# Kernel tuning notes

Measured on AMD Instinct MI355X. Metric: run time of the kernel, lower is better.

The kernel has to match this reference:

```python
import jax, jax.numpy as jnp
import numpy as np

ALPHA = 0.2          # LeakyReLU negative slope
NEG_BIG = -9e15      # mask fill value from the original code
N, IN_F, OUT_F = 8192, 128, 64


def setup_inputs() -> dict:
    key = jax.random.key(0)
    k1, k2, k3, k4 = jax.random.split(key, 4)
    h = jax.random.normal(k1, (N, IN_F), dtype=jnp.float32)
    adj = jax.random.randint(k2, (N, N), 0, 2, dtype=jnp.int32)
    W = jax.random.normal(k3, (IN_F, OUT_F), dtype=jnp.float32) * 0.1
    a = jax.random.normal(k4, (2 * OUT_F, 1), dtype=jnp.float32) * 0.1
    return {"h": h, "adj": adj, "W": W, "a": a}


def reference(h, adj, W, a):
    # Wh: [N, F]
    Wh = h @ W
    # e_ij = leakyrelu([Wh_i ; Wh_j] . a) = leakyrelu(Wh_i.a1 + Wh_j.a2)
    # (identical math to the original NxNx2F concat, without materializing it)
    a1 = a[:OUT_F, 0]   # [F]
    a2 = a[OUT_F:, 0]   # [F]
    s1 = Wh @ a1        # [N]
    s2 = Wh @ a2        # [N]
    e = jax.nn.leaky_relu(s1[:, None] + s2[None, :], negative_slope=ALPHA)  # [N, N]
    e = jnp.where(adj > 0, e, jnp.float32(NEG_BIG))
    attention = jax.nn.softmax(e, axis=1)
    # dropout is identity at inference (training=False)
    h_prime = attention @ Wh  # [N, F]
    return jax.nn.elu(h_prime)  # concat=True -> elu
```

## Files before the change

kernel.cpp:

```cpp
#include <hip/hip_runtime.h>
#include <hip/hip_bf16.h>

#define N 8192
#define IN_F 128
#define OUT_F 64
#define LRELU_ALPHA 0.2f
#define PAD 520

typedef __attribute__((ext_vector_type(8))) short short8;
typedef __attribute__((ext_vector_type(4))) float float4v;
typedef __attribute__((ext_vector_type(4))) unsigned short ushortx4;

__device__ __forceinline__ unsigned short bf16_bits(float x) {
  unsigned u = __builtin_bit_cast(unsigned, x);
  u += 0x7fffu + ((u >> 16) & 1u);
  return (unsigned short)(u >> 16);
}

__global__ __launch_bounds__(256) void prep_kernel(
    const float* __restrict__ h, const float* __restrict__ W,
    const float* __restrict__ a, float* __restrict__ s1,
    float* __restrict__ s2, unsigned short* __restrict__ whT) {
  const int tid = threadIdx.x;
  const int row = blockIdx.x * 4 + (tid >> 6);
  const int k = tid & 63;
  const float* hr = h + row * IN_F;
  float acc = 0.f;
#pragma unroll 8
  for (int c = 0; c < IN_F; ++c) acc = fmaf(hr[c], W[c * OUT_F + k], acc);
  whT[(long)k * N + row] = bf16_bits(acc);
  float p1 = acc * a[k];
  float p2 = acc * a[OUT_F + k];
#pragma unroll
  for (int off = 32; off > 0; off >>= 1) {
    p1 += __shfl_xor(p1, off);
    p2 += __shfl_xor(p2, off);
  }
  if (k == 0) { s1[row] = p1; s2[row] = p2; }
}

__global__ __launch_bounds__(256) void repack_kernel(
    const unsigned short* __restrict__ whT, unsigned short* __restrict__ whF) {
  const int f = blockIdx.x * 256 + threadIdx.x;
  const int lane = f & 63, tt = (f >> 6) & 3, c = f >> 8;
  const int r16 = lane & 15, quad = lane >> 4;
  const short8 v = *(const short8*)(whT + (long)(tt * 16 + r16) * N + c * 32 + quad * 8);
  *(short8*)(whF + (long)f * 8) = v;
}

__device__ __forceinline__ void p_write(unsigned short* pr, int c, int4 av,
                                        float4 s2v, float s1w) {
  float e0 = s1w + s2v.x; e0 = fmaxf(e0, LRELU_ALPHA * e0);
  float e1 = s1w + s2v.y; e1 = fmaxf(e1, LRELU_ALPHA * e1);
  float e2 = s1w + s2v.z; e2 = fmaxf(e2, LRELU_ALPHA * e2);
  float e3 = s1w + s2v.w; e3 = fmaxf(e3, LRELU_ALPHA * e3);
  const float p0 = av.x > 0 ? __expf(e0) : 0.f;
  const float p1 = av.y > 0 ? __expf(e1) : 0.f;
  const float p2 = av.z > 0 ? __expf(e2) : 0.f;
  const float p3 = av.w > 0 ? __expf(e3) : 0.f;
  ushortx4 pk = {bf16_bits(p0), bf16_bits(p1), bf16_bits(p2), bf16_bits(p3)};
  *(ushortx4*)(pr + c) = pk;
}

__global__ __launch_bounds__(1024, 4) void gat_kernel(
    const int* __restrict__ adj, const float* __restrict__ s1,
    const float* __restrict__ s2, const unsigned short* __restrict__ whF,
    float* __restrict__ out) {
  __shared__ __align__(16) unsigned short pbuf[2][16][PAD];
  const int tid = threadIdx.x;
  const int w = tid >> 6, L = tid & 63;
  const int r16 = L & 15, quad = L >> 4;
  const int row0 = blockIdx.x * 16;
  const long arow = (long)(row0 + w) * N;
  const float s1w = s1[row0 + w];

  float4v acc0 = {0.f, 0.f, 0.f, 0.f};
  float4v acc1 = {0.f, 0.f, 0.f, 0.f};
  float4v acc2 = {0.f, 0.f, 0.f, 0.f};
  float4v acc3 = {0.f, 0.f, 0.f, 0.f};
  float4v accD = {0.f, 0.f, 0.f, 0.f};
  const short ONE = (short)0x3F80;
  const short8 ones = {ONE, ONE, ONE, ONE, ONE, ONE, ONE, ONE};

  {
    const int c = L * 4;
    const int4 a0 = *(const int4*)(adj + arow + c);
    const int4 a1 = *(const int4*)(adj + arow + 256 + c);
    const float4 sv0 = *(const float4*)(s2 + c);
    const float4 sv1 = *(const float4*)(s2 + 256 + c);
    p_write(pbuf[0][w], c, a0, sv0, s1w);
    p_write(pbuf[0][w], 256 + c, a1, sv1, s1w);
  }
  __syncthreads();

  for (int it = 0; it < 16; ++it) {
    const int b = it & 1;
    int4 na0, na1;
    float4 ns0, ns1;
    if (it < 15) {
      const long base = arow + (it + 1) * 512 + L * 4;
      na0 = *(const int4*)(adj + base);
      na1 = *(const int4*)(adj + base + 256);
      ns0 = *(const float4*)(s2 + (it + 1) * 512 + L * 4);
      ns1 = *(const float4*)(s2 + (it + 1) * 512 + 256 + L * 4);
    }
    const int c32 = it * 16 + w;
    const short8 afrag = *(const short8*)(&pbuf[b][r16][w * 32 + quad * 8]);
    const unsigned short* bp = whF + ((long)c32 * 256 + L) * 8;
    const short8 b0 = *(const short8*)(bp);
    const short8 b1 = *(const short8*)(bp + 512);
    const short8 b2 = *(const short8*)(bp + 1024);
    const short8 b3 = *(const short8*)(bp + 1536);
    acc0 = __builtin_amdgcn_mfma_f32_16x16x32_bf16(afrag, b0, acc0, 0, 0, 0);
    acc1 = __builtin_amdgcn_mfma_f32_16x16x32_bf16(afrag, b1, acc1, 0, 0, 0);
    acc2 = __builtin_amdgcn_mfma_f32_16x16x32_bf16(afrag, b2, acc2, 0, 0, 0);
    acc3 = __builtin_amdgcn_mfma_f32_16x16x32_bf16(afrag, b3, acc3, 0, 0, 0);
    accD = __builtin_amdgcn_mfma_f32_16x16x32_bf16(afrag, ones, accD, 0, 0, 0);
    if (it < 15) {
      unsigned short* pr = pbuf[b ^ 1][w];
      const int c = L * 4;
      p_write(pr, c, na0, ns0, s1w);
      p_write(pr, 256 + c, na1, ns1, s1w);
    }
    __syncthreads();
  }

  float* M = (float*)pbuf;
  if (w >= 8) {
    float* S = M + (w - 8) * 1040;
#pragma unroll
    for (int reg = 0; reg < 4; ++reg) {
      const int r = quad * 4 + reg;
      S[r * 64 + 0 * 16 + r16] = acc0[reg];
      S[r * 64 + 1 * 16 + r16] = acc1[reg];
      S[r * 64 + 2 * 16 + r16] = acc2[reg];
      S[r * 64 + 3 * 16 + r16] = acc3[reg];
      if (r16 == 0) S[1024 + r] = accD[reg];
    }
  }
  __syncthreads();
  if (w < 8) {
    float* S = M + w * 1040;
#pragma unroll
    for (int reg = 0; reg < 4; ++reg) {
      const int r = quad * 4 + reg;
      S[r * 64 + 0 * 16 + r16] += acc0[reg];
      S[r * 64 + 1 * 16 + r16] += acc1[reg];
      S[r * 64 + 2 * 16 + r16] += acc2[reg];
      S[r * 64 + 3 * 16 + r16] += acc3[reg];
      if (r16 == 0) S[1024 + r] += accD[reg];
    }
  }
  __syncthreads();
  {
    const int r = tid >> 6, k = tid & 63;
    float Sv = 0.f, Lv = 0.f;
#pragma unroll
    for (int s = 0; s < 8; ++s) {
      Sv += M[s * 1040 + r * 64 + k];
      Lv += M[s * 1040 + 1024 + r];
    }
    const float v = Sv / Lv;
    out[(long)(row0 + r) * OUT_F + k] = v > 0.f ? v : expm1f(v);
  }
}

extern "C" void kernel_launch(void* const* d_in, const int* in_sizes, int n_in,
                              void* d_out, int out_size, void* d_ws, size_t ws_size,
                              hipStream_t stream) {
  const float* h = (const float*)d_in[0];
  const int* adj = (const int*)d_in[1];
  const float* W = (const float*)d_in[2];
  const float* a = (const float*)d_in[3];
  float* out = (float*)d_out;

  float* s1 = (float*)d_ws;
  float* s2 = s1 + N;
  unsigned short* whT = (unsigned short*)(s2 + N);
  unsigned short* whF = whT + (long)OUT_F * N;

  prep_kernel<<<N / 4, 256, 0, stream>>>(h, W, a, s1, s2, whT);
  repack_kernel<<<N * OUT_F / 8 / 256, 256, 0, stream>>>(whT, whF);
  gat_kernel<<<N / 16, 1024, 0, stream>>>(adj, s1, s2, whF, out);
}
```

Baseline: 392.1 us.

## Halve gat block size, two rows per wave, deeper adj prefetch

The GAT kernel now launches 512 threads per block, and each wave handles two attention rows and two K-chunks per iteration. Adjacency loads are prefetched two iterations ahead through a register ring so more HBM traffic is in flight per wave. The final reduction across waves is adapted to 8 waves with 4 partial slices. The prep kernel also reads h rows as float4. The cost is more live registers per thread, which may lower occupancy.

```diff
diff --git a/kernel.cpp b/kernel.cpp
--- a/kernel.cpp
+++ b/kernel.cpp
@@ -24,10 +24,17 @@
   const int tid = threadIdx.x;
   const int row = blockIdx.x * 4 + (tid >> 6);
   const int k = tid & 63;
-  const float* hr = h + row * IN_F;
+  const float4* hr4 = (const float4*)(h + row * IN_F);
   float acc = 0.f;
-#pragma unroll 8
-  for (int c = 0; c < IN_F; ++c) acc = fmaf(hr[c], W[c * OUT_F + k], acc);
+#pragma unroll
+  for (int c4 = 0; c4 < IN_F / 4; ++c4) {
+    const float4 hv = hr4[c4];
+    const int cb = c4 * 4;
+    acc = fmaf(hv.x, W[(cb + 0) * OUT_F + k], acc);
+    acc = fmaf(hv.y, W[(cb + 1) * OUT_F + k], acc);
+    acc = fmaf(hv.z, W[(cb + 2) * OUT_F + k], acc);
+    acc = fmaf(hv.w, W[(cb + 3) * OUT_F + k], acc);
+  }
   whT[(long)k * N + row] = bf16_bits(acc);
   float p1 = acc * a[k];
   float p2 = acc * a[OUT_F + k];
@@ -62,7 +69,7 @@
   *(ushortx4*)(pr + c) = pk;
 }
 
-__global__ __launch_bounds__(1024, 4) void gat_kernel(
+__global__ __launch_bounds__(512, 4) void gat_kernel(
     const int* __restrict__ adj, const float* __restrict__ s1,
     const float* __restrict__ s2, const unsigned short* __restrict__ whF,
     float* __restrict__ out) {
@@ -71,8 +78,12 @@
   const int w = tid >> 6, L = tid & 63;
   const int r16 = L & 15, quad = L >> 4;
   const int row0 = blockIdx.x * 16;
-  const long arow = (long)(row0 + w) * N;
-  const float s1w = s1[row0 + w];
+  const int rA = 2 * w, rB = 2 * w + 1;
+  const long arowA = (long)(row0 + rA) * N;
+  const long arowB = (long)(row0 + rB) * N;
+  const float s1A = s1[row0 + rA];
+  const float s1B = s1[row0 + rB];
+  const int c = L * 4;
 
   float4v acc0 = {0.f, 0.f, 0.f, 0.f};
   float4v acc1 = {0.f, 0.f, 0.f, 0.f};
@@ -82,52 +93,77 @@
   const short ONE = (short)0x3F80;
   const short8 ones = {ONE, ONE, ONE, ONE, ONE, ONE, ONE, ONE};
 
+  int4 pA0[2], pA1[2], pB0[2], pB1[2];
+  float4 ps0, ps1;
+
   {
-    const int c = L * 4;
-    const int4 a0 = *(const int4*)(adj + arow + c);
-    const int4 a1 = *(const int4*)(adj + arow + 256 + c);
+    const int4 a0 = *(const int4*)(adj + arowA + c);
+    const int4 a1 = *(const int4*)(adj + arowA + 256 + c);
+    const int4 b0 = *(const int4*)(adj + arowB + c);
+    const int4 b1 = *(const int4*)(adj + arowB + 256 + c);
     const float4 sv0 = *(const float4*)(s2 + c);
     const float4 sv1 = *(const float4*)(s2 + 256 + c);
-    p_write(pbuf[0][w], c, a0, sv0, s1w);
-    p_write(pbuf[0][w], 256 + c, a1, sv1, s1w);
+    pA0[0] = *(const int4*)(adj + arowA + 512 + c);
+    pA1[0] = *(const int4*)(adj + arowA + 512 + 256 + c);
+    pB0[0] = *(const int4*)(adj + arowB + 512 + c);
+    pB1[0] = *(const int4*)(adj + arowB + 512 + 256 + c);
+    pA0[1] = *(const int4*)(adj + arowA + 1024 + c);
+    pA1[1] = *(const int4*)(adj + arowA + 1024 + 256 + c);
+    pB0[1] = *(const int4*)(adj + arowB + 1024 + c);
+    pB1[1] = *(const int4*)(adj + arowB + 1024 + 256 + c);
+    ps0 = *(const float4*)(s2 + 512 + c);
+    ps1 = *(const float4*)(s2 + 512 + 256 + c);
+    p_write(pbuf[0][rA], c, a0, sv0, s1A);
+    p_write(pbuf[0][rA], 256 + c, a1, sv1, s1A);
+    p_write(pbuf[0][rB], c, b0, sv0, s1B);
+    p_write(pbuf[0][rB], 256 + c, b1, sv1, s1B);
   }
   __syncthreads();
 
+#pragma unroll
   for (int it = 0; it < 16; ++it) {
     const int b = it & 1;
-    int4 na0, na1;
-    float4 ns0, ns1;
+    const int s = it & 1;
+#pragma unroll
+    for (int half = 0; half < 2; ++half) {
+      const int cc = w + half * 8;
+      const short8 afrag = *(const short8*)(&pbuf[b][r16][cc * 32 + quad * 8]);
+      const unsigned short* bp = whF + ((long)(it * 16 + cc) * 256 + L) * 8;
+      const short8 b0 = *(const short8*)(bp);
+      const short8 b1 = *(const short8*)(bp + 512);
+      const short8 b2 = *(const short8*)(bp + 1024);
+      const short8 b3 = *(const short8*)(bp + 1536);
+      acc0 = __builtin_amdgcn_mfma_f32_16x16x32_bf16(afrag, b0, acc0, 0, 0, 0);
+      acc1 = __builtin_amdgcn_mfma_f32_16x16x32_bf16(afrag, b1, acc1, 0, 0, 0);
+      acc2 = __builtin_amdgcn_mfma_f32_16x16x32_bf16(afrag, b2, acc2, 0, 0, 0);
+      acc3 = __builtin_amdgcn_mfma_f32_16x16x32_bf16(afrag, b3, acc3, 0, 0, 0);
+      accD = __builtin_amdgcn_mfma_f32_16x16x32_bf16(afrag, ones, accD, 0, 0, 0);
+    }
     if (it < 15) {
-      const long base = arow + (it + 1) * 512 + L * 4;
-      na0 = *(const int4*)(adj + base);
-      na1 = *(const int4*)(adj + base + 256);
-      ns0 = *(const float4*)(s2 + (it + 1) * 512 + L * 4);
-      ns1 = *(const float4*)(s2 + (it + 1) * 512 + 256 + L * 4);
-    }
-    const int c32 = it * 16 + w;
-    const short8 afrag = *(const short8*)(&pbuf[b][r16][w * 32 + quad * 8]);
-    const unsigned short* bp = whF + ((long)c32 * 256 + L) * 8;
-    const short8 b0 = *(const short8*)(bp);
-    const short8 b1 = *(const short8*)(bp + 512);
-    const short8 b2 = *(const short8*)(bp + 1024);
-    const short8 b3 = *(const short8*)(bp + 1536);
-    acc0 = __builtin_amdgcn_mfma_f32_16x16x32_bf16(afrag, b0, acc0, 0, 0, 0);
-    acc1 = __builtin_amdgcn_mfma_f32_16x16x32_bf16(afrag, b1, acc1, 0, 0, 0);
-    acc2 = __builtin_amdgcn_mfma_f32_16x16x32_bf16(afrag, b2, acc2, 0, 0, 0);
-    acc3 = __builtin_amdgcn_mfma_f32_16x16x32_bf16(afrag, b3, acc3, 0, 0, 0);
-    accD = __builtin_amdgcn_mfma_f32_16x16x32_bf16(afrag, ones, accD, 0, 0, 0);
-    if (it < 15) {
-      unsigned short* pr = pbuf[b ^ 1][w];
-      const int c = L * 4;
-      p_write(pr, c, na0, ns0, s1w);
-      p_write(pr, 256 + c, na1, ns1, s1w);
+      unsigned short* prA = pbuf[b ^ 1][rA];
+      unsigned short* prB = pbuf[b ^ 1][rB];
+      p_write(prA, c, pA0[s], ps0, s1A);
+      p_write(prA, 256 + c, pA1[s], ps1, s1A);
+      p_write(prB, c, pB0[s], ps0, s1B);
+      p_write(prB, 256 + c, pB1[s], ps1, s1B);
+      if (it < 13) {
+        const long base = (long)(it + 3) * 512 + c;
+        pA0[s] = *(const int4*)(adj + arowA + base);
+        pA1[s] = *(const int4*)(adj + arowA + base + 256);
+        pB0[s] = *(const int4*)(adj + arowB + base);
+        pB1[s] = *(const int4*)(adj + arowB + base + 256);
+      }
+      if (it < 14) {
+        ps0 = *(const float4*)(s2 + (it + 2) * 512 + c);
+        ps1 = *(const float4*)(s2 + (it + 2) * 512 + 256 + c);
+      }
     }
     __syncthreads();
   }
 
   float* M = (float*)pbuf;
-  if (w >= 8) {
-    float* S = M + (w - 8) * 1040;
+  if (w >= 4) {
+    float* S = M + (w - 4) * 1040;
 #pragma unroll
     for (int reg = 0; reg < 4; ++reg) {
       const int r = quad * 4 + reg;
@@ -139,7 +175,7 @@
     }
   }
   __syncthreads();
-  if (w < 8) {
+  if (w < 4) {
     float* S = M + w * 1040;
 #pragma unroll
     for (int reg = 0; reg < 4; ++reg) {
@@ -152,13 +188,15 @@
     }
   }
   __syncthreads();
-  {
-    const int r = tid >> 6, k = tid & 63;
+#pragma unroll
+  for (int part = 0; part < 2; ++part) {
+    const int e = part * 512 + tid;
+    const int r = e >> 6, k = e & 63;
     float Sv = 0.f, Lv = 0.f;
 #pragma unroll
-    for (int s = 0; s < 8; ++s) {
-      Sv += M[s * 1040 + r * 64 + k];
-      Lv += M[s * 1040 + 1024 + r];
+    for (int sl = 0; sl < 4; ++sl) {
+      Sv += M[sl * 1040 + r * 64 + k];
+      Lv += M[sl * 1040 + 1024 + r];
     }
     const float v = Sv / Lv;
     out[(long)(row0 + r) * OUT_F + k] = v > 0.f ? v : expm1f(v);
@@ -181,5 +219,5 @@
 
   prep_kernel<<<N / 4, 256, 0, stream>>>(h, W, a, s1, s2, whT);
   repack_kernel<<<N * OUT_F / 8 / 256, 256, 0, stream>>>(whT, whF);
-  gat_kernel<<<N / 16, 1024, 0, stream>>>(adj, s1, s2, whF, out);
-}
+  gat_kernel<<<N / 16, 512, 0, stream>>>(adj, s1, s2, whF, out);
+}
```

After: 394.6 us. About the same (+0.6%).
